# Optimization experiments

Hardware: AMD Instinct MI355X
Metric: run time of the kernel (lower is better)

## Reference

```python
import jax, jax.numpy as jnp
import numpy as np
from jax.ops import segment_sum

NUM_EMBEDDINGS = 512
EMBEDDING_DIM = 64
COMMITMENT_COST = 0.25
DECAY = 0.99
EPSILON = 1e-05


def setup_inputs() -> dict:
    key = jax.random.key(0)
    k1, k2, k3 = jax.random.split(key, 3)
    B, C, T = 32, EMBEDDING_DIM, 4096
    z = jax.random.normal(k1, (B, C, T), dtype=jnp.float32)
    embedding = jax.random.normal(k2, (NUM_EMBEDDINGS, EMBEDDING_DIM), dtype=jnp.float32)
    cluster_size = jnp.zeros((NUM_EMBEDDINGS,), dtype=jnp.float32)
    embed_avg = jax.random.normal(k3, (NUM_EMBEDDINGS, EMBEDDING_DIM), dtype=jnp.float32)
    return {"z": z, "embedding": embedding, "cluster_size": cluster_size, "embed_avg": embed_avg}


def reference(z, embedding, cluster_size, embed_avg):
    B, C, T = z.shape
    K = embedding.shape[0]
    # flatten: (B, C, T) -> (B*T, C), matching reshape(B,C,-1).permute(0,2,1).reshape(-1,C)
    z_flat = jnp.transpose(z, (0, 2, 1)).reshape(-1, C)  # [N, C]
    N = z_flat.shape[0]

    # squared-euclidean nearest-code search (argmin of cdist == argmin of sq dist)
    d2 = (jnp.sum(z_flat * z_flat, axis=1, keepdims=True)
          - 2.0 * (z_flat @ embedding.T)
          + jnp.sum(embedding * embedding, axis=1)[None, :])  # [N, K]
    indices = jnp.argmin(d2, axis=1)  # [N] int

    # quantize: gather instead of one-hot matmul (same math)
    quantized_flat = embedding[indices]  # [N, C]
    quantized = jnp.transpose(quantized_flat.reshape(B, T, C), (0, 2, 1))  # [B, C, T]

    # EMA codebook update (training branch)
    n = segment_sum(jnp.ones((N,), dtype=z.dtype), indices, num_segments=K)  # [K]
    new_cluster_size = cluster_size * DECAY + (1.0 - DECAY) * n
    embed_sum = segment_sum(z_flat, indices, num_segments=K)  # [K, C]
    new_embed_avg = embed_avg * DECAY + (1.0 - DECAY) * embed_sum
    n_tot = jnp.sum(new_cluster_size)
    cs_smoothed = (new_cluster_size + EPSILON) / (n_tot + K * EPSILON) * n_tot
    new_embedding = new_embed_avg / cs_smoothed[:, None]

    # commitment loss against detached quantized
    commitment_loss = jnp.mean((z - jax.lax.stop_gradient(quantized)) ** 2)
    vq_loss = COMMITMENT_COST * commitment_loss

    # straight-through estimator
    quantized_st = z + jax.lax.stop_gradient(quantized - z)

    # perplexity over code usage (zero-count codes contribute ~0, as in torch unique version)
    probs = n / N
    perplexity = jnp.exp(-jnp.sum(probs * jnp.log(probs + 1e-10)))

    return (quantized_st, indices, vq_loss, perplexity,
            new_embedding, new_cluster_size, new_embed_avg)
```

## Files before the change

### kernel.cpp

```cpp
#include <hip/hip_runtime.h>
#include <math.h>

#define KB_NUM 512
#define DIMC 64
#define BSZ 32
#define TLEN 4096
#define NTOK (BSZ * TLEN)
#define DECAY_F 0.99f
#define EPS_F 1e-5f
#define NPART 256

#define Q_OFF    ((size_t)0)
#define IDX_OFF  ((size_t)BSZ * DIMC * TLEN)
#define LOSS_OFF (IDX_OFF + (size_t)NTOK)
#define PLEX_OFF (LOSS_OFF + 1)
#define NEMB_OFF (PLEX_OFF + 1)
#define NCS_OFF  (NEMB_OFF + (size_t)KB_NUM * DIMC)
#define NEA_OFF  (NCS_OFF + (size_t)KB_NUM)

typedef _Float16 f16x8 __attribute__((ext_vector_type(8)));
typedef float    f32x4 __attribute__((ext_vector_type(4)));

__global__ __launch_bounds__(64) void vq_prep_e(
    const float* __restrict__ emb,
    _Float16* __restrict__ efrag,
    float* __restrict__ enorm)
{
    const int k = blockIdx.x;
    const int c = threadIdx.x;
    float v = emb[(size_t)k * DIMC + c];
    _Float16 h = (_Float16)v;
    _Float16 l = (_Float16)(v - (float)h);

    const int kgrp = k >> 4, row = k & 15;
    const int ks = c >> 5, seg = (c & 31) >> 3, j = c & 7;
    const int lane = seg * 16 + row;
    const size_t base = ((size_t)(kgrp * 2 + ks) * 2) * 512;
    efrag[base + (size_t)lane * 8 + j]       = h;
    efrag[base + 512 + (size_t)lane * 8 + j] = l;

    float s = v * v;
    #pragma unroll
    for (int off = 32; off > 0; off >>= 1)
        s += __shfl_down(s, off, 64);
    if (c == 0) enorm[k] = 0.5f * s;
}

#define LOADA(P, kg) do {                                                     \
    const _Float16* fb_ = efrag + ((size_t)((kg) & 31) * 4) * 512             \
                                + (size_t)ln * 8;                             \
    P##h0 = *(const f16x8*)(fb_);                                             \
    P##l0 = *(const f16x8*)(fb_ + 512);                                       \
    P##h1 = *(const f16x8*)(fb_ + 1024);                                      \
    P##l1 = *(const f16x8*)(fb_ + 1536);                                      \
} while (0)

#define CONSUME(P, ct) do {                                                   \
    _Pragma("unroll")                                                         \
    for (int tt = 0; tt < 4; ++tt)                                            \
        acc[ct][tt] = __builtin_amdgcn_mfma_f32_16x16x32_f16(                 \
            P##h0, zhf[tt][0], acc[ct][tt], 0, 0, 0);                         \
    _Pragma("unroll")                                                         \
    for (int tt = 0; tt < 4; ++tt)                                            \
        acc[ct][tt] = __builtin_amdgcn_mfma_f32_16x16x32_f16(                 \
            P##h0, zlf[tt][0], acc[ct][tt], 0, 0, 0);                         \
    _Pragma("unroll")                                                         \
    for (int tt = 0; tt < 4; ++tt)                                            \
        acc[ct][tt] = __builtin_amdgcn_mfma_f32_16x16x32_f16(                 \
            P##l0, zhf[tt][0], acc[ct][tt], 0, 0, 0);                         \
    _Pragma("unroll")                                                         \
    for (int tt = 0; tt < 4; ++tt)                                            \
        acc[ct][tt] = __builtin_amdgcn_mfma_f32_16x16x32_f16(                 \
            P##l0, zlf[tt][0], acc[ct][tt], 0, 0, 0);                         \
    _Pragma("unroll")                                                         \
    for (int tt = 0; tt < 4; ++tt)                                            \
        acc[ct][tt] = __builtin_amdgcn_mfma_f32_16x16x32_f16(                 \
            P##h1, zhf[tt][1], acc[ct][tt], 0, 0, 0);                         \
    _Pragma("unroll")                                                         \
    for (int tt = 0; tt < 4; ++tt)                                            \
        acc[ct][tt] = __builtin_amdgcn_mfma_f32_16x16x32_f16(                 \
            P##h1, zlf[tt][1], acc[ct][tt], 0, 0, 0);                         \
    _Pragma("unroll")                                                         \
    for (int tt = 0; tt < 4; ++tt)                                            \
        acc[ct][tt] = __builtin_amdgcn_mfma_f32_16x16x32_f16(                 \
            P##l1, zhf[tt][1], acc[ct][tt], 0, 0, 0);                         \
    _Pragma("unroll")                                                         \
    for (int tt = 0; tt < 4; ++tt)                                            \
        acc[ct][tt] = __builtin_amdgcn_mfma_f32_16x16x32_f16(                 \
            P##l1, zlf[tt][1], acc[ct][tt], 0, 0, 0);                         \
} while (0)

__global__ __launch_bounds__(256, 2) void vq_main_kernel(
    const float* __restrict__ z,
    const float* __restrict__ emb,
    const _Float16* __restrict__ efrag,
    const float* __restrict__ enorm,
    float* __restrict__ out,
    float* __restrict__ lossAcc)
{
    __shared__ float zs[256 * 65];
    __shared__ float sen[KB_NUM];

    const int tid = threadIdx.x;
    const int w   = tid >> 6;
    const int ln  = tid & 63;
    const int bk  = blockIdx.x;
    const int b   = bk >> 4;
    const int t0  = (bk & 15) << 8;

    sen[tid]       = enorm[tid];
    sen[tid + 256] = enorm[tid + 256];

    const float* zg = z + (size_t)b * (DIMC * TLEN) + t0;

    #pragma unroll 8
    for (int c = 0; c < DIMC; ++c)
        zs[tid * 65 + c] = zg[(size_t)c * TLEN + tid];
    __syncthreads();

    f16x8 zhf[4][2], zlf[4][2];
    #pragma unroll
    for (int tt = 0; tt < 4; ++tt) {
        #pragma unroll
        for (int ks = 0; ks < 2; ++ks) {
            const float* zrow = &zs[(w * 64 + tt * 16 + (ln & 15)) * 65
                                    + ks * 32 + ((ln >> 4) << 3)];
            #pragma unroll
            for (int j = 0; j < 8; ++j) {
                float v = zrow[j];
                _Float16 h = (_Float16)v;
                zhf[tt][ks][j] = h;
                zlf[tt][ks][j] = (_Float16)(v - (float)h);
            }
        }
    }

    float bv[4] = {3.4e38f, 3.4e38f, 3.4e38f, 3.4e38f};
    int   bi[4] = {0, 0, 0, 0};

    f16x8 A0h0, A0l0, A0h1, A0l1;
    f16x8 A1h0, A1l0, A1h1, A1l1;
    LOADA(A0, 0);
    LOADA(A1, 1);

    #pragma unroll 1
    for (int chunk = 0; chunk < 8; ++chunk) {
        const int kb = chunk * 4;
        f32x4 acc[4][4];
        #pragma unroll
        for (int ct = 0; ct < 4; ++ct)
            #pragma unroll
            for (int tt = 0; tt < 4; ++tt)
                acc[ct][tt] = (f32x4){0.f, 0.f, 0.f, 0.f};

        CONSUME(A0, 0); LOADA(A0, kb + 2);
        CONSUME(A1, 1); LOADA(A1, kb + 3);
        CONSUME(A0, 2); LOADA(A0, kb + 4);
        CONSUME(A1, 3); LOADA(A1, kb + 5);

        #pragma unroll
        for (int ct = 0; ct < 4; ++ct) {
            const int cb = chunk * 64 + ct * 16 + ((ln >> 4) << 2);
            float4 en = *(const float4*)&sen[cb];
            const float e0 = en.x, e1 = en.y, e2 = en.z, e3 = en.w;
            #pragma unroll
            for (int tt = 0; tt < 4; ++tt) {
                float s0 = e0 - acc[ct][tt][0];
                float s1 = e1 - acc[ct][tt][1];
                float s2 = e2 - acc[ct][tt][2];
                float s3 = e3 - acc[ct][tt][3];
                if (s0 < bv[tt]) { bv[tt] = s0; bi[tt] = cb; }
                if (s1 < bv[tt]) { bv[tt] = s1; bi[tt] = cb + 1; }
                if (s2 < bv[tt]) { bv[tt] = s2; bi[tt] = cb + 2; }
                if (s3 < bv[tt]) { bv[tt] = s3; bi[tt] = cb + 3; }
            }
        }
    }

    #pragma unroll
    for (int mask = 16; mask <= 32; mask <<= 1) {
        #pragma unroll
        for (int tt = 0; tt < 4; ++tt) {
            float ov = __shfl_xor(bv[tt], mask, 64);
            int   oi = __shfl_xor(bi[tt], mask, 64);
            if (ov < bv[tt] || (ov == bv[tt] && oi < bi[tt])) {
                bv[tt] = ov; bi[tt] = oi;
            }
        }
    }

    const int g = ln >> 4;
    const int idxv = (g == 0) ? bi[0] : (g == 1) ? bi[1] : (g == 2) ? bi[2] : bi[3];
    const int tok = w * 64 + ln;

    out[IDX_OFF + (size_t)b * TLEN + t0 + tok] = (float)idxv;

    const float* er   = emb + (size_t)idxv * DIMC;
    const float* zrow = &zs[tok * 65];
    float* qo = out + (size_t)b * (DIMC * TLEN) + t0 + tok;

    float lsum = 0.f;
    #pragma unroll
    for (int c4 = 0; c4 < DIMC / 4; ++c4) {
        float4 ev = *(const float4*)(er + c4 * 4);
        float z0 = zrow[c4 * 4 + 0], z1 = zrow[c4 * 4 + 1];
        float z2 = zrow[c4 * 4 + 2], z3 = zrow[c4 * 4 + 3];
        float d0 = ev.x - z0, d1 = ev.y - z1, d2 = ev.z - z2, d3 = ev.w - z3;
        qo[(size_t)(c4 * 4 + 0) * TLEN] = z0 + d0;
        qo[(size_t)(c4 * 4 + 1) * TLEN] = z1 + d1;
        qo[(size_t)(c4 * 4 + 2) * TLEN] = z2 + d2;
        qo[(size_t)(c4 * 4 + 3) * TLEN] = z3 + d3;
        lsum = fmaf(d0, d0, lsum); lsum = fmaf(d1, d1, lsum);
        lsum = fmaf(d2, d2, lsum); lsum = fmaf(d3, d3, lsum);
    }

    #pragma unroll
    for (int off = 32; off > 0; off >>= 1)
        lsum += __shfl_down(lsum, off, 64);
    if (ln == 0) atomicAdd(lossAcc, lsum);
}

template <bool ATOMICFLUSH>
__global__ __launch_bounds__(512, 1) void vq_bin_kernel(
    const float* __restrict__ z,
    const float* __restrict__ out,
    float* __restrict__ pcnt,
    float* __restrict__ pesum)
{
    __shared__ float accT[DIMC][KB_NUM + 1];
    __shared__ float scnt[KB_NUM];

    const int tid = threadIdx.x;
    for (int j = tid; j < DIMC * (KB_NUM + 1); j += 512) ((float*)accT)[j] = 0.f;
    scnt[tid] = 0.f;
    __syncthreads();

    const int b  = blockIdx.x >> 3;
    const int tb = (blockIdx.x & 7) * 512;
    const int myidx = (int)out[IDX_OFF + (size_t)b * TLEN + tb + tid];
    atomicAdd(&scnt[myidx], 1.0f);

    const float* zp = z + (size_t)b * (DIMC * TLEN) + tb;
    #pragma unroll 8
    for (int c = 0; c < DIMC; ++c) {
        float v = zp[(size_t)c * TLEN + tid];
        atomicAdd(&accT[c][myidx], v);
    }
    __syncthreads();

    float* pe = pesum + (size_t)blockIdx.x * (KB_NUM * DIMC);
    for (int j = tid; j < KB_NUM * DIMC; j += 512) {
        const int k = j >> 6, c = j & 63;
        float v = accT[c][k];
        if (ATOMICFLUSH) { if (v != 0.f) atomicAdd(pe + j, v); }
        else             pe[j] = v;
    }
    if (ATOMICFLUSH) {
        float v = scnt[tid];
        if (v != 0.f) atomicAdd(pcnt + tid, v);
    } else {
        pcnt[(size_t)blockIdx.x * KB_NUM + tid] = scnt[tid];
    }
}

__global__ __launch_bounds__(512) void vq_stats_kernel(
    const float* __restrict__ cluster_size,
    const float* __restrict__ pcnt,
    const float* __restrict__ lossAcc,
    float* __restrict__ out,
    float* __restrict__ ntotp,
    int P)
{
    __shared__ float part[4][KB_NUM];
    __shared__ float red[KB_NUM];

    const int tid = threadIdx.x;
    const int pg  = tid >> 7;
    const int kq  = tid & 127;

    {
        const int pcount = (P + 3) / 4;
        const int p0 = pg * pcount;
        float4 a = {0.f, 0.f, 0.f, 0.f};
        for (int p = p0; p < p0 + pcount && p < P; ++p) {
            float4 v = *(const float4*)(pcnt + (size_t)p * KB_NUM + kq * 4);
            a.x += v.x; a.y += v.y; a.z += v.z; a.w += v.w;
        }
        part[pg][kq * 4 + 0] = a.x;
        part[pg][kq * 4 + 1] = a.y;
        part[pg][kq * 4 + 2] = a.z;
        part[pg][kq * 4 + 3] = a.w;
    }
    __syncthreads();

    const int k = tid;
    float n = part[0][k] + part[1][k] + part[2][k] + part[3][k];

    float ncs = cluster_size[k] * DECAY_F + (1.0f - DECAY_F) * n;
    out[NCS_OFF + k] = ncs;

    red[k] = ncs;
    __syncthreads();
    for (int s = KB_NUM / 2; s > 0; s >>= 1) {
        if (k < s) red[k] += red[k + s];
        __syncthreads();
    }
    if (k == 0) ntotp[0] = red[0];
    __syncthreads();

    float p = n * (1.0f / (float)NTOK);
    red[k] = p * logf(p + 1e-10f);
    __syncthreads();
    for (int s = KB_NUM / 2; s > 0; s >>= 1) {
        if (k < s) red[k] += red[k + s];
        __syncthreads();
    }
    if (k == 0) {
        out[PLEX_OFF] = expf(-red[0]);
        out[LOSS_OFF] = 0.25f * lossAcc[0] * (1.0f / (float)(BSZ * DIMC * TLEN));
    }
}

__global__ __launch_bounds__(256) void vq_embed_kernel(
    const float* __restrict__ embed_avg,
    const float* __restrict__ pesum,
    const float* __restrict__ ntotp,
    float* __restrict__ out,
    int P)
{
    const int j = blockIdx.x * 256 + threadIdx.x;
    const int k = j >> 6;

    float e0 = 0.f, e1 = 0.f, e2 = 0.f, e3 = 0.f;
    int p = 0;
    #pragma unroll 4
    for (; p + 4 <= P; p += 4) {
        e0 += pesum[(size_t)(p + 0) * (KB_NUM * DIMC) + j];
        e1 += pesum[(size_t)(p + 1) * (KB_NUM * DIMC) + j];
        e2 += pesum[(size_t)(p + 2) * (KB_NUM * DIMC) + j];
        e3 += pesum[(size_t)(p + 3) * (KB_NUM * DIMC) + j];
    }
    for (; p < P; ++p) e0 += pesum[(size_t)p * (KB_NUM * DIMC) + j];
    float es = (e0 + e1) + (e2 + e3);

    float nea = embed_avg[j] * DECAY_F + (1.0f - DECAY_F) * es;
    out[NEA_OFF + j] = nea;

    float ncs  = out[NCS_OFF + k];
    float ntot = ntotp[0];
    float denom = (ncs + EPS_F) / (ntot + (float)KB_NUM * EPS_F) * ntot;
    out[NEMB_OFF + j] = nea / denom;
}

extern "C" void kernel_launch(void* const* d_in, const int* in_sizes, int n_in,
                              void* d_out, int out_size, void* d_ws, size_t ws_size,
                              hipStream_t stream)
{
    const float* z            = (const float*)d_in[0];
    const float* emb          = (const float*)d_in[1];
    const float* cluster_size = (const float*)d_in[2];
    const float* embed_avg    = (const float*)d_in[3];
    float* out = (float*)d_out;

    char* ws = (char*)d_ws;
    float*     lossAcc = (float*)ws;
    float*     ntotp   = (float*)(ws + 64);
    float*     enorm   = (float*)(ws + 256);
    _Float16*  efrag   = (_Float16*)(ws + 4096);
    const size_t PART_OFF   = 4096 + 131072;
    const size_t pcnt_bytes  = (size_t)NPART * KB_NUM * sizeof(float);
    const size_t pesum_bytes = (size_t)NPART * KB_NUM * DIMC * sizeof(float);
    const size_t need = PART_OFF + pcnt_bytes + pesum_bytes;

    int P;
    float *pcnt, *pesum;
    if (ws_size >= need) {
        P = NPART;
        pcnt  = (float*)(ws + PART_OFF);
        pesum = (float*)(ws + PART_OFF + pcnt_bytes);
        hipMemsetAsync(ws, 0, 4096, stream);
    } else {
        P = 1;
        pcnt  = (float*)(ws + PART_OFF);
        pesum = (float*)(ws + PART_OFF + KB_NUM * sizeof(float));
        hipMemsetAsync(ws, 0, PART_OFF + (KB_NUM + KB_NUM * DIMC) * sizeof(float),
                       stream);
    }

    vq_prep_e<<<dim3(KB_NUM), dim3(DIMC), 0, stream>>>(emb, efrag, enorm);

    vq_main_kernel<<<dim3(NTOK / 256), dim3(256), 0, stream>>>(
        z, emb, efrag, enorm, out, lossAcc);

    if (P == NPART)
        vq_bin_kernel<false><<<dim3(NTOK / 512), dim3(512), 0, stream>>>(
            z, out, pcnt, pesum);
    else
        vq_bin_kernel<true><<<dim3(NTOK / 512), dim3(512), 0, stream>>>(
            z, out, pcnt, pesum);

    vq_stats_kernel<<<dim3(1), dim3(512), 0, stream>>>(
        cluster_size, pcnt, lossAcc, out, ntotp, P);

    vq_embed_kernel<<<dim3(KB_NUM * DIMC / 256), dim3(256), 0, stream>>>(
        embed_avg, pesum, ntotp, out, P);
}
```

Before: 151.9 us.

## Split codebook binning across four blocks per chunk to shrink LDS and raise occupancy

The binning kernel now splits the 512 codes into four quarters of 128. Each of four blocks per token chunk accumulates only the tokens whose index falls in its quarter, which cuts shared memory from about 130KB to about 33KB and allows several blocks per CU. Partial counts are stored transposed so the stats kernel can sum each code's row with contiguous float4 loads, and the embed kernel reads the new quarter-major layout. The cost is that every block re-reads z and the indices for its chunk, so global z traffic in this stage goes up fourfold.

Result: slower. 155.2 us (+2.2%).

```diff
diff --git a/kernel.cpp b/kernel.cpp
--- a/kernel.cpp
+++ b/kernel.cpp
@@ -8,7 +8,8 @@
 #define NTOK (BSZ * TLEN)
 #define DECAY_F 0.99f
 #define EPS_F 1e-5f
-#define NPART 256
+#define NCHUNK 256
+#define KQ 128
 
 #define Q_OFF    ((size_t)0)
 #define IDX_OFF  ((size_t)BSZ * DIMC * TLEN)
@@ -221,80 +222,84 @@
 }
 
 template <bool ATOMICFLUSH>
-__global__ __launch_bounds__(512, 1) void vq_bin_kernel(
+__global__ __launch_bounds__(512, 4) void vq_bin_kernel(
     const float* __restrict__ z,
     const float* __restrict__ out,
-    float* __restrict__ pcnt,
-    float* __restrict__ pesum)
-{
-    __shared__ float accT[DIMC][KB_NUM + 1];
-    __shared__ float scnt[KB_NUM];
-
-    const int tid = threadIdx.x;
-    for (int j = tid; j < DIMC * (KB_NUM + 1); j += 512) ((float*)accT)[j] = 0.f;
-    scnt[tid] = 0.f;
-    __syncthreads();
-
-    const int b  = blockIdx.x >> 3;
-    const int tb = (blockIdx.x & 7) * 512;
-    const int myidx = (int)out[IDX_OFF + (size_t)b * TLEN + tb + tid];
-    atomicAdd(&scnt[myidx], 1.0f);
+    float* __restrict__ pcntT,
+    float* __restrict__ pesum,
+    int P)
+{
+    __shared__ float acc[KQ][DIMC + 1];
+    __shared__ float scnt[KQ];
+
+    const int tid   = threadIdx.x;
+    const int chunk = blockIdx.x >> 2;
+    const int q     = blockIdx.x & 3;
+
+    for (int j = tid; j < KQ * (DIMC + 1); j += 512) ((float*)acc)[j] = 0.f;
+    if (tid < KQ) scnt[tid] = 0.f;
+    __syncthreads();
+
+    const int b  = chunk >> 3;
+    const int tb = (chunk & 7) * 512;
+    const int myidx  = (int)out[IDX_OFF + (size_t)b * TLEN + tb + tid];
+    const bool owned = (myidx >> 7) == q;
+    const int klocal = myidx & (KQ - 1);
+    if (owned) atomicAdd(&scnt[klocal], 1.0f);
 
     const float* zp = z + (size_t)b * (DIMC * TLEN) + tb;
     #pragma unroll 8
     for (int c = 0; c < DIMC; ++c) {
         float v = zp[(size_t)c * TLEN + tid];
-        atomicAdd(&accT[c][myidx], v);
-    }
-    __syncthreads();
-
-    float* pe = pesum + (size_t)blockIdx.x * (KB_NUM * DIMC);
-    for (int j = tid; j < KB_NUM * DIMC; j += 512) {
+        if (owned) atomicAdd(&acc[klocal][c], v);
+    }
+    __syncthreads();
+
+    const int pidx = (ATOMICFLUSH ? 0 : chunk);
+    float* pe = pesum + ((size_t)q * P + pidx) * (KQ * DIMC);
+    for (int j = tid; j < KQ * DIMC; j += 512) {
         const int k = j >> 6, c = j & 63;
-        float v = accT[c][k];
+        float v = acc[k][c];
         if (ATOMICFLUSH) { if (v != 0.f) atomicAdd(pe + j, v); }
         else             pe[j] = v;
     }
-    if (ATOMICFLUSH) {
+    if (tid < KQ) {
         float v = scnt[tid];
-        if (v != 0.f) atomicAdd(pcnt + tid, v);
-    } else {
-        pcnt[(size_t)blockIdx.x * KB_NUM + tid] = scnt[tid];
+        if (ATOMICFLUSH) { if (v != 0.f) atomicAdd(pcntT + (size_t)(q * KQ + tid) * P, v); }
+        else             pcntT[(size_t)(q * KQ + tid) * P + pidx] = v;
     }
 }
 
 __global__ __launch_bounds__(512) void vq_stats_kernel(
     const float* __restrict__ cluster_size,
-    const float* __restrict__ pcnt,
+    const float* __restrict__ pcntT,
     const float* __restrict__ lossAcc,
     float* __restrict__ out,
     float* __restrict__ ntotp,
     int P)
 {
-    __shared__ float part[4][KB_NUM];
     __shared__ float red[KB_NUM];
-
-    const int tid = threadIdx.x;
-    const int pg  = tid >> 7;
-    const int kq  = tid & 127;
-
-    {
-        const int pcount = (P + 3) / 4;
-        const int p0 = pg * pcount;
-        float4 a = {0.f, 0.f, 0.f, 0.f};
-        for (int p = p0; p < p0 + pcount && p < P; ++p) {
-            float4 v = *(const float4*)(pcnt + (size_t)p * KB_NUM + kq * 4);
-            a.x += v.x; a.y += v.y; a.z += v.z; a.w += v.w;
+    const int k = threadIdx.x;
+
+    float n = 0.f;
+    if (P >= 4) {
+        const float4* row = (const float4*)(pcntT + (size_t)k * P);
+        float4 a0 = {0,0,0,0}, a1 = {0,0,0,0};
+        int p4 = 0;
+        #pragma unroll 4
+        for (; p4 + 2 <= P / 4; p4 += 2) {
+            float4 v0 = row[p4], v1 = row[p4 + 1];
+            a0.x += v0.x; a0.y += v0.y; a0.z += v0.z; a0.w += v0.w;
+            a1.x += v1.x; a1.y += v1.y; a1.z += v1.z; a1.w += v1.w;
         }
-        part[pg][kq * 4 + 0] = a.x;
-        part[pg][kq * 4 + 1] = a.y;
-        part[pg][kq * 4 + 2] = a.z;
-        part[pg][kq * 4 + 3] = a.w;
-    }
-    __syncthreads();
-
-    const int k = tid;
-    float n = part[0][k] + part[1][k] + part[2][k] + part[3][k];
+        for (; p4 < P / 4; ++p4) {
+            float4 v0 = row[p4];
+            a0.x += v0.x; a0.y += v0.y; a0.z += v0.z; a0.w += v0.w;
+        }
+        n = ((a0.x + a0.y) + (a0.z + a0.w)) + ((a1.x + a1.y) + (a1.z + a1.w));
+    } else {
+        n = pcntT[(size_t)k * P];
+    }
 
     float ncs = cluster_size[k] * DECAY_F + (1.0f - DECAY_F) * n;
     out[NCS_OFF + k] = ncs;
@@ -330,17 +335,20 @@
 {
     const int j = blockIdx.x * 256 + threadIdx.x;
     const int k = j >> 6;
-
+    const int q = j >> 13;
+    const int rem = j & 8191;
+
+    const float* base = pesum + (size_t)q * P * (KQ * DIMC) + rem;
     float e0 = 0.f, e1 = 0.f, e2 = 0.f, e3 = 0.f;
     int p = 0;
     #pragma unroll 4
     for (; p + 4 <= P; p += 4) {
-        e0 += pesum[(size_t)(p + 0) * (KB_NUM * DIMC) + j];
-        e1 += pesum[(size_t)(p + 1) * (KB_NUM * DIMC) + j];
-        e2 += pesum[(size_t)(p + 2) * (KB_NUM * DIMC) + j];
-        e3 += pesum[(size_t)(p + 3) * (KB_NUM * DIMC) + j];
-    }
-    for (; p < P; ++p) e0 += pesum[(size_t)p * (KB_NUM * DIMC) + j];
+        e0 += base[(size_t)(p + 0) * (KQ * DIMC)];
+        e1 += base[(size_t)(p + 1) * (KQ * DIMC)];
+        e2 += base[(size_t)(p + 2) * (KQ * DIMC)];
+        e3 += base[(size_t)(p + 3) * (KQ * DIMC)];
+    }
+    for (; p < P; ++p) e0 += base[(size_t)p * (KQ * DIMC)];
     float es = (e0 + e1) + (e2 + e3);
 
     float nea = embed_avg[j] * DECAY_F + (1.0f - DECAY_F) * es;
@@ -367,23 +375,24 @@
     float*     ntotp   = (float*)(ws + 64);
     float*     enorm   = (float*)(ws + 256);
     _Float16*  efrag   = (_Float16*)(ws + 4096);
-    const size_t PART_OFF   = 4096 + 131072;
-    const size_t pcnt_bytes  = (size_t)NPART * KB_NUM * sizeof(float);
-    const size_t pesum_bytes = (size_t)NPART * KB_NUM * DIMC * sizeof(float);
-    const size_t need = PART_OFF + pcnt_bytes + pesum_bytes;
+    const size_t PART_OFF = 4096 + 131072;
+
+    const size_t pcntT_full = (size_t)KB_NUM * NCHUNK * sizeof(float);
+    const size_t pesum_full = (size_t)4 * NCHUNK * KQ * DIMC * sizeof(float);
+    const size_t need = PART_OFF + pcntT_full + pesum_full;
 
     int P;
-    float *pcnt, *pesum;
+    float *pcntT, *pesum;
     if (ws_size >= need) {
-        P = NPART;
-        pcnt  = (float*)(ws + PART_OFF);
-        pesum = (float*)(ws + PART_OFF + pcnt_bytes);
+        P = NCHUNK;
+        pcntT = (float*)(ws + PART_OFF);
+        pesum = (float*)(ws + PART_OFF + pcntT_full);
         hipMemsetAsync(ws, 0, 4096, stream);
     } else {
         P = 1;
-        pcnt  = (float*)(ws + PART_OFF);
+        pcntT = (float*)(ws + PART_OFF);
         pesum = (float*)(ws + PART_OFF + KB_NUM * sizeof(float));
-        hipMemsetAsync(ws, 0, PART_OFF + (KB_NUM + KB_NUM * DIMC) * sizeof(float),
+        hipMemsetAsync(ws, 0, PART_OFF + (KB_NUM + 4 * KQ * DIMC) * sizeof(float),
                        stream);
     }
 
@@ -392,15 +401,15 @@
     vq_main_kernel<<<dim3(NTOK / 256), dim3(256), 0, stream>>>(
         z, emb, efrag, enorm, out, lossAcc);
 
-    if (P == NPART)
-        vq_bin_kernel<false><<<dim3(NTOK / 512), dim3(512), 0, stream>>>(
-            z, out, pcnt, pesum);
+    if (P == NCHUNK)
+        vq_bin_kernel<false><<<dim3(NCHUNK * 4), dim3(512), 0, stream>>>(
+            z, out, pcntT, pesum, P);
     else
-        vq_bin_kernel<true><<<dim3(NTOK / 512), dim3(512), 0, stream>>>(
-            z, out, pcnt, pesum);
+        vq_bin_kernel<true><<<dim3(NCHUNK * 4), dim3(512), 0, stream>>>(
+            z, out, pcntT, pesum, P);
 
     vq_stats_kernel<<<dim3(1), dim3(512), 0, stream>>>(
-        cluster_size, pcnt, lossAcc, out, ntotp, P);
+        cluster_size, pcntT, lossAcc, out, ntotp, P);
 
     vq_embed_kernel<<<dim3(KB_NUM * DIMC / 256), dim3(256), 0, stream>>>(
         embed_avg, pesum, ntotp, out, P);
```
